# Optimization experiments

Hardware: AMD Instinct MI355X
Metric: run time of the kernel (lower is better)

## Reference

```python
import jax, jax.numpy as jnp
import numpy as np

DT = 0.01
DT_SCALE = 1.0

B, D, R = 4096, 1024, 256

def setup_inputs() -> dict:
    key = jax.random.key(0)
    kx, kv, kf, ku, kw = jax.random.split(key, 5)
    x = jax.random.normal(kx, (B, D), dtype=jnp.float32)
    v = jax.random.normal(kv, (B, D), dtype=jnp.float32)
    force = jax.random.normal(kf, (B, D), dtype=jnp.float32)
    # low-rank Christoffel factors; scaled down so the quadratic term stays stable
    U = jax.random.normal(ku, (D, R), dtype=jnp.float32) * (1.0 / np.sqrt(D))
    W = jax.random.normal(kw, (R, D), dtype=jnp.float32) * (1.0 / np.sqrt(R))
    return {"x": x, "v": v, "force": force, "U": U, "W": W, "steps": 8}

def christoffel(v, U, W):
    # Gamma(v, v) = ((v @ U) ** 2) @ W  -- factored quadratic form
    p = v @ U            # [B, R]
    return (p * p) @ W   # [B, D]

def reference(x, v, force, U, W, steps):
    dt = DT * DT_SCALE

    def step(carry, _):
        cx, cv = carry
        acc = force - christoffel(cv, U, W)
        cx = cx + dt * cv
        cv = cv + dt * acc
        return (cx, cv), None

    (cx, cv), _ = jax.lax.scan(step, (x, v), None, length=steps)
    return (cx, cv)
```

## Files before the change

### kernel.cpp

```cpp
#include <hip/hip_runtime.h>


#define BB 4096
#define DD 1024
#define RR 256
#define DT 0.01f

typedef __attribute__((ext_vector_type(8))) short short8;
typedef __attribute__((ext_vector_type(4))) short short4v;
typedef __attribute__((ext_vector_type(4))) float floatx4;

static __device__ inline unsigned short f2bf(float f) {
    union { float f; unsigned int u; } c; c.f = f;
    unsigned int u = c.u;
    u += 0x7fffu + ((u >> 16) & 1u);
    return (unsigned short)(u >> 16);
}

__global__ __launch_bounds__(1024)
void pack_kernel(const float* __restrict__ U, const float* __restrict__ W,
                 short* __restrict__ Up, short* __restrict__ Wp,
                 short* __restrict__ WUp) {
    __shared__ float4 red[16][64];
    const int b = blockIdx.x;
    const int tid = threadIdx.x;

    if (b < 128) {
        const bool isU = (b < 64);
        const float* M = isU ? U : W;
        short* P = isU ? Up : Wp;
        const int ld = isU ? RR : DD;
        int t = (isU ? b : b - 64) * 1024 + tid;
        int S = t * 4;
        int j0   = S & 7;
        int lane = (S >> 3) & 63;
        int frag = S >> 9;
        int nl = lane & 15, kq = lane >> 4;
        int kt, nt;
        if (isU) { kt = frag >> 4; nt = frag & 15; }
        else     { kt = frag >> 6; nt = frag & 63; }
        int k0 = kt * 32 + kq * 8 + j0;
        int n  = nt * 16 + nl;
        short4v o;
#pragma unroll
        for (int jj = 0; jj < 4; jj++)
            o[jj] = (short)f2bf(M[(long)(k0 + jj) * ld + n]);
        *(short4v*)(P + S) = o;
    } else {
        const int i  = b - 128;
        const int ks = tid >> 6;
        const int j4 = tid & 63;
        const float4* U4 = (const float4*)U;
        const float*  wr = W + (long)i * DD + ks * 64;
        float4 acc = {0.f, 0.f, 0.f, 0.f};
#pragma unroll 8
        for (int m = 0; m < 64; m++) {
            float w = wr[m];
            float4 u = U4[(ks * 64 + m) * 64 + j4];
            acc.x += w * u.x; acc.y += w * u.y;
            acc.z += w * u.z; acc.w += w * u.w;
        }
        red[ks][j4] = acc;
        __syncthreads();
        if (tid < 64) {
            float4 a = red[0][tid];
#pragma unroll
            for (int s = 1; s < 16; s++) {
                float4 r = red[s][tid];
                a.x += r.x; a.y += r.y; a.z += r.z; a.w += r.w;
            }
            int ktw = i >> 5, kqw = (i >> 3) & 3, jjw = i & 7;
            float av[4] = {a.x, a.y, a.z, a.w};
#pragma unroll
            for (int c = 0; c < 4; c++) {
                int j = 4 * tid + c;
                int nt = j >> 4, nl = j & 15;
                WUp[(((ktw * 16 + nt) * 64) + kqw * 16 + nl) * 8 + jjw] =
                    (short)f2bf(av[c]);
            }
        }
    }
}

__global__ __launch_bounds__(1024)
void euler_kernel(const float* __restrict__ x0,
                  const float* __restrict__ v0,
                  const float* __restrict__ force,
                  const short8* __restrict__ Up,
                  const short8* __restrict__ Wp,
                  const short8* __restrict__ WUp,
                  const int* __restrict__ steps_p,
                  float* __restrict__ out) {
    __shared__ __align__(16) short smem[74240];

    const int tid  = threadIdx.x;
    const int wave = tid >> 6;
    const int lane = tid & 63;
    const int nl   = lane & 15;
    const int quad = lane >> 4;
    const int row0 = blockIdx.x * 16;
    const int steps = steps_p[0];
    const float sdt  = steps * DT;
    const float tdt2 = 0.5f * (float)(steps * (steps - 1)) * DT * DT;

    short (*va)[1032] = (short(*)[1032])smem;
    short (*fa)[1032] = (short(*)[1032])(smem + 16512);
    short (*q1)[264]  = (short(*)[264])(smem + 33024);
    short (*q2)[264]  = (short(*)[264])(smem + 37248);

    const float4* v04 = (const float4*)v0;
    const float4* f44 = (const float4*)force;
    const float4* x4  = (const float4*)x0;
    float4 e1[4], e2[4];
#pragma unroll
    for (int i = 0; i < 4; i++) {
        int idx = tid + i * 1024;
        int row = idx >> 8, c4 = idx & 255;
        long g = (long)(row0 + row) * 256 + c4;
        float4 vv = v04[g];
        float4 ff = f44[g];
        float4 xx = x4[g];
        short4v sv, sf;
        sv[0] = (short)f2bf(vv.x); sv[1] = (short)f2bf(vv.y);
        sv[2] = (short)f2bf(vv.z); sv[3] = (short)f2bf(vv.w);
        sf[0] = (short)f2bf(ff.x); sf[1] = (short)f2bf(ff.y);
        sf[2] = (short)f2bf(ff.z); sf[3] = (short)f2bf(ff.w);
        *(short4v*)&va[row][c4 * 4] = sv;
        *(short4v*)&fa[row][c4 * 4] = sf;
        e1[i].x = xx.x + sdt * vv.x + tdt2 * ff.x;
        e1[i].y = xx.y + sdt * vv.y + tdt2 * ff.y;
        e1[i].z = xx.z + sdt * vv.z + tdt2 * ff.z;
        e1[i].w = xx.w + sdt * vv.w + tdt2 * ff.w;
        e2[i].x = vv.x + sdt * ff.x;
        e2[i].y = vv.y + sdt * ff.y;
        e2[i].z = vv.z + sdt * ff.z;
        e2[i].w = vv.w + sdt * ff.w;
    }

    short8 wu[8];
#pragma unroll
    for (int kt = 0; kt < 8; kt++)
        wu[kt] = WUp[(kt * 16 + wave) * 64 + lane];

    __syncthreads();

    floatx4 P  = {0.f, 0.f, 0.f, 0.f};
    floatx4 FU = {0.f, 0.f, 0.f, 0.f};
#pragma unroll 4
    for (int kt = 0; kt < 32; kt++) {
        short8 av = *(const short8*)&va[nl][kt * 32 + quad * 8];
        short8 af = *(const short8*)&fa[nl][kt * 32 + quad * 8];
        short8 bu = Up[(kt * 16 + wave) * 64 + lane];
        P  = __builtin_amdgcn_mfma_f32_16x16x32_bf16(av, bu, P,  0, 0, 0);
        FU = __builtin_amdgcn_mfma_f32_16x16x32_bf16(af, bu, FU, 0, 0, 0);
    }

    floatx4 A1 = {0.f, 0.f, 0.f, 0.f};
    floatx4 Q2 = {0.f, 0.f, 0.f, 0.f};
    for (int s = 0; s < steps; s++) {
        short (*pw)[264] = (s & 1) ? q2 : q1;
        float wgt = (float)(steps - 1 - s);
#pragma unroll
        for (int r = 0; r < 4; r++) {
            float g = P[r] * P[r];
            A1[r] += g;
            Q2[r] += wgt * g;
            pw[4 * quad + r][16 * wave + nl] = (short)f2bf(g);
        }
        __syncthreads();
        floatx4 acc = {0.f, 0.f, 0.f, 0.f};
#pragma unroll
        for (int kt = 0; kt < 8; kt++) {
            short8 a = *(const short8*)&pw[nl][kt * 32 + quad * 8];
            acc = __builtin_amdgcn_mfma_f32_16x16x32_bf16(a, wu[kt], acc, 0, 0, 0);
        }
#pragma unroll
        for (int r = 0; r < 4; r++)
            P[r] += DT * (FU[r] - acc[r]);
    }
    __syncthreads();

#pragma unroll
    for (int r = 0; r < 4; r++) {
        q1[4 * quad + r][16 * wave + nl] = (short)f2bf(A1[r]);
        q2[4 * quad + r][16 * wave + nl] = (short)f2bf(Q2[r]);
    }
    __syncthreads();

    floatx4 y1[4], y2[4];
#pragma unroll
    for (int t = 0; t < 4; t++) {
        y1[t] = (floatx4){0.f, 0.f, 0.f, 0.f};
        y2[t] = (floatx4){0.f, 0.f, 0.f, 0.f};
    }
#pragma unroll 2
    for (int kt = 0; kt < 8; kt++) {
        short8 a1 = *(const short8*)&q1[nl][kt * 32 + quad * 8];
        short8 a2 = *(const short8*)&q2[nl][kt * 32 + quad * 8];
#pragma unroll
        for (int t = 0; t < 4; t++) {
            short8 b = Wp[(kt * 64 + 4 * wave + t) * 64 + lane];
            y1[t] = __builtin_amdgcn_mfma_f32_16x16x32_bf16(a1, b, y1[t], 0, 0, 0);
            y2[t] = __builtin_amdgcn_mfma_f32_16x16x32_bf16(a2, b, y2[t], 0, 0, 0);
        }
    }

    float (*s1)[1024] = (float(*)[1024])smem;
    float (*s2)[1024] = (float(*)[1024])(smem + 41472);
#pragma unroll
    for (int t = 0; t < 4; t++) {
        int col = 64 * wave + 16 * t + nl;
#pragma unroll
        for (int r = 0; r < 4; r++) {
            int row = 4 * quad + r;
            s1[row][col] = -DT * y1[t][r];
            s2[row][col] = -DT * DT * y2[t][r];
        }
    }
    __syncthreads();

    float4* out4 = (float4*)out;
#pragma unroll
    for (int p = 0; p < 4; p++) {
        int idx = tid + p * 1024;
        int row = idx >> 8, c4 = idx & 255;
        long gi = (long)(row0 + row) * 256 + c4;
        float4 t1 = *(const float4*)&s1[row][c4 * 4];
        float4 t2 = *(const float4*)&s2[row][c4 * 4];
        float4 ox, ov;
        ox.x = e1[p].x + t2.x;  ox.y = e1[p].y + t2.y;
        ox.z = e1[p].z + t2.z;  ox.w = e1[p].w + t2.w;
        ov.x = e2[p].x + t1.x;  ov.y = e2[p].y + t1.y;
        ov.z = e2[p].z + t1.z;  ov.w = e2[p].w + t1.w;
        out4[gi] = ox;
        out4[(long)BB * 256 + gi] = ov;
    }
}

extern "C" void kernel_launch(void* const* d_in, const int* in_sizes, int n_in,
                              void* d_out, int out_size, void* d_ws, size_t ws_size,
                              hipStream_t stream) {
    const float* x     = (const float*)d_in[0];
    const float* v     = (const float*)d_in[1];
    const float* force = (const float*)d_in[2];
    const float* U     = (const float*)d_in[3];
    const float* W     = (const float*)d_in[4];
    const int*   steps = (const int*)d_in[5];

    short* Up  = (short*)d_ws;
    short* Wp  = Up + 262144;
    short* WUp = Wp + 262144;

    pack_kernel<<<384, 1024, 0, stream>>>(U, W, Up, Wp, WUp);
    euler_kernel<<<256, 1024, 0, stream>>>(x, v, force,
                                           (const short8*)Up, (const short8*)Wp,
                                           (const short8*)WUp,
                                           steps, (float*)d_out);
}
```

Baseline: 149.3 us.

## Halve rows per block to double grid and cut register pressure

```diff
diff --git a/kernel.cpp b/kernel.cpp
--- a/kernel.cpp
+++ b/kernel.cpp
@@ -82,7 +82,7 @@
     }
 }
 
-__global__ __launch_bounds__(1024)
+__global__ __launch_bounds__(1024, 8)
 void euler_kernel(const float* __restrict__ x0,
                   const float* __restrict__ v0,
                   const float* __restrict__ force,
@@ -91,35 +91,30 @@
                   const short8* __restrict__ WUp,
                   const int* __restrict__ steps_p,
                   float* __restrict__ out) {
-    __shared__ __align__(16) short smem[74240];
+    __shared__ __align__(16) short smem[32768];
 
     const int tid  = threadIdx.x;
     const int wave = tid >> 6;
     const int lane = tid & 63;
     const int nl   = lane & 15;
     const int quad = lane >> 4;
-    const int row0 = blockIdx.x * 16;
+    const int row0 = blockIdx.x * 8;
     const int steps = steps_p[0];
-    const float sdt  = steps * DT;
-    const float tdt2 = 0.5f * (float)(steps * (steps - 1)) * DT * DT;
 
     short (*va)[1032] = (short(*)[1032])smem;
-    short (*fa)[1032] = (short(*)[1032])(smem + 16512);
-    short (*q1)[264]  = (short(*)[264])(smem + 33024);
-    short (*q2)[264]  = (short(*)[264])(smem + 37248);
+    short (*fa)[1032] = (short(*)[1032])(smem + 8256);
+    short (*q1)[264]  = (short(*)[264])(smem + 16512);
+    short (*q2)[264]  = (short(*)[264])(smem + 20736);
 
     const float4* v04 = (const float4*)v0;
     const float4* f44 = (const float4*)force;
-    const float4* x4  = (const float4*)x0;
-    float4 e1[4], e2[4];
-#pragma unroll
-    for (int i = 0; i < 4; i++) {
+#pragma unroll
+    for (int i = 0; i < 2; i++) {
         int idx = tid + i * 1024;
         int row = idx >> 8, c4 = idx & 255;
         long g = (long)(row0 + row) * 256 + c4;
         float4 vv = v04[g];
         float4 ff = f44[g];
-        float4 xx = x4[g];
         short4v sv, sf;
         sv[0] = (short)f2bf(vv.x); sv[1] = (short)f2bf(vv.y);
         sv[2] = (short)f2bf(vv.z); sv[3] = (short)f2bf(vv.w);
@@ -127,21 +122,7 @@
         sf[2] = (short)f2bf(ff.z); sf[3] = (short)f2bf(ff.w);
         *(short4v*)&va[row][c4 * 4] = sv;
         *(short4v*)&fa[row][c4 * 4] = sf;
-        e1[i].x = xx.x + sdt * vv.x + tdt2 * ff.x;
-        e1[i].y = xx.y + sdt * vv.y + tdt2 * ff.y;
-        e1[i].z = xx.z + sdt * vv.z + tdt2 * ff.z;
-        e1[i].w = xx.w + sdt * vv.w + tdt2 * ff.w;
-        e2[i].x = vv.x + sdt * ff.x;
-        e2[i].y = vv.y + sdt * ff.y;
-        e2[i].z = vv.z + sdt * ff.z;
-        e2[i].w = vv.w + sdt * ff.w;
-    }
-
-    short8 wu[8];
-#pragma unroll
-    for (int kt = 0; kt < 8; kt++)
-        wu[kt] = WUp[(kt * 16 + wave) * 64 + lane];
-
+    }
     __syncthreads();
 
     floatx4 P  = {0.f, 0.f, 0.f, 0.f};
@@ -155,6 +136,11 @@
         FU = __builtin_amdgcn_mfma_f32_16x16x32_bf16(af, bu, FU, 0, 0, 0);
     }
 
+    short8 wu[8];
+#pragma unroll
+    for (int kt = 0; kt < 8; kt++)
+        wu[kt] = WUp[(kt * 16 + wave) * 64 + lane];
+
     floatx4 A1 = {0.f, 0.f, 0.f, 0.f};
     floatx4 Q2 = {0.f, 0.f, 0.f, 0.f};
     for (int s = 0; s < steps; s++) {
@@ -204,34 +190,47 @@
             y2[t] = __builtin_amdgcn_mfma_f32_16x16x32_bf16(a2, b, y2[t], 0, 0, 0);
         }
     }
+    __syncthreads();
 
     float (*s1)[1024] = (float(*)[1024])smem;
-    float (*s2)[1024] = (float(*)[1024])(smem + 41472);
-#pragma unroll
-    for (int t = 0; t < 4; t++) {
-        int col = 64 * wave + 16 * t + nl;
-#pragma unroll
-        for (int r = 0; r < 4; r++) {
-            int row = 4 * quad + r;
-            s1[row][col] = -DT * y1[t][r];
-            s2[row][col] = -DT * DT * y2[t][r];
-        }
-    }
-    __syncthreads();
-
+    float (*s2)[1024] = (float(*)[1024])(smem + 16384);
+    if (quad < 2) {
+#pragma unroll
+        for (int t = 0; t < 4; t++) {
+            int col = 64 * wave + 16 * t + nl;
+#pragma unroll
+            for (int r = 0; r < 4; r++) {
+                int row = 4 * quad + r;
+                s1[row][col] = -DT * y1[t][r];
+                s2[row][col] = -DT * DT * y2[t][r];
+            }
+        }
+    }
+    __syncthreads();
+
+    const float sdt  = steps * DT;
+    const float tdt2 = 0.5f * (float)(steps * (steps - 1)) * DT * DT;
+    const float4* x4 = (const float4*)x0;
     float4* out4 = (float4*)out;
 #pragma unroll
-    for (int p = 0; p < 4; p++) {
+    for (int p = 0; p < 2; p++) {
         int idx = tid + p * 1024;
         int row = idx >> 8, c4 = idx & 255;
         long gi = (long)(row0 + row) * 256 + c4;
+        float4 xx = x4[gi];
+        float4 vv = v04[gi];
+        float4 ff = f44[gi];
         float4 t1 = *(const float4*)&s1[row][c4 * 4];
         float4 t2 = *(const float4*)&s2[row][c4 * 4];
         float4 ox, ov;
-        ox.x = e1[p].x + t2.x;  ox.y = e1[p].y + t2.y;
-        ox.z = e1[p].z + t2.z;  ox.w = e1[p].w + t2.w;
-        ov.x = e2[p].x + t1.x;  ov.y = e2[p].y + t1.y;
-        ov.z = e2[p].z + t1.z;  ov.w = e2[p].w + t1.w;
+        ox.x = xx.x + sdt * vv.x + tdt2 * ff.x + t2.x;
+        ox.y = xx.y + sdt * vv.y + tdt2 * ff.y + t2.y;
+        ox.z = xx.z + sdt * vv.z + tdt2 * ff.z + t2.z;
+        ox.w = xx.w + sdt * vv.w + tdt2 * ff.w + t2.w;
+        ov.x = vv.x + sdt * ff.x + t1.x;
+        ov.y = vv.y + sdt * ff.y + t1.y;
+        ov.z = vv.z + sdt * ff.z + t1.z;
+        ov.w = vv.w + sdt * ff.w + t1.w;
         out4[gi] = ox;
         out4[(long)BB * 256 + gi] = ov;
     }
@@ -252,7 +251,7 @@
     short* WUp = Wp + 262144;
 
     pack_kernel<<<384, 1024, 0, stream>>>(U, W, Up, Wp, WUp);
-    euler_kernel<<<256, 1024, 0, stream>>>(x, v, force,
+    euler_kernel<<<512, 1024, 0, stream>>>(x, v, force,
                                            (const short8*)Up, (const short8*)Wp,
                                            (const short8*)WUp,
                                            steps, (float*)d_out);
```

After: 179.3 us. 1.2x slower.
